# Optimization experiments

Measured on AMD Instinct MI355X. Metric: run time of the kernel, lower is better.

The kernel has to match this reference:

```python
import jax, jax.numpy as jnp
import numpy as np

N, F, B, T, K, C = 1000, 64, 16, 12, 5, 10
E = 16 * N
LN_EPS = 1e-5


def setup_inputs() -> dict:
    key = jax.random.key(0)
    ks = jax.random.split(key, 12)
    x = jax.random.normal(ks[0], (B, T, N, F), jnp.float32)
    # Edge list: ring guarantees every node has in-degree and out-degree >= 1
    # (DConv takes reciprocal of degrees), plus random edges to avg degree 16.
    rng = np.random.default_rng(0)
    ring = np.arange(N)
    src = np.concatenate([ring, rng.integers(0, N, E - N)])
    dst = np.concatenate([(ring + 1) % N, rng.integers(0, N, E - N)])
    edge_index = jnp.asarray(np.stack([src, dst]), jnp.int32)

    def winit(k, shape, fan):
        return (jax.random.normal(k, shape, jnp.float32) / np.sqrt(fan)).astype(jnp.float32)

    # DCRNN GRU cell = 3 diffusion convs, each on concat([X, H]) (2F in-channels)
    # DConv weight shape: (2 directions, K, in_channels, out_channels)
    W_z = winit(ks[1], (2, K, 2 * F, F), 2 * F)
    W_r = winit(ks[2], (2, K, 2 * F, F), 2 * F)
    W_h = winit(ks[3], (2, K, 2 * F, F), 2 * F)
    b_z = winit(ks[4], (F,), 100)
    b_r = winit(ks[5], (F,), 100)
    b_h = winit(ks[6], (F,), 100)
    ln_g = jnp.ones((F,), jnp.float32)
    ln_b = jnp.zeros((F,), jnp.float32)
    lin_w = winit(ks[7], (C, T * N * F), T * N * F)
    lin_b = winit(ks[8], (C,), 100)
    return {"x": x, "edge_index": edge_index, "W_z": W_z, "b_z": b_z,
            "W_r": W_r, "b_r": b_r, "W_h": W_h, "b_h": b_h,
            "ln_g": ln_g, "ln_b": ln_b, "lin_w": lin_w, "lin_b": lin_b}


def reference(x, edge_index, W_z, b_z, W_r, b_r, W_h, b_h, ln_g, ln_b, lin_w, lin_b):
    row, col = edge_index[0], edge_index[1]
    ones = jnp.ones(row.shape[0], x.dtype)
    deg_out = jax.ops.segment_sum(ones, row, num_segments=N)  # out-degree of src
    deg_in = jax.ops.segment_sum(ones, col, num_segments=N)   # in-degree (col sums)
    norm_out = (1.0 / deg_out)[row]  # per-edge 1/deg_out[src]
    norm_in = (1.0 / deg_in)[row]    # per-edge 1/deg_in[src] (src = target of reversed edge)

    def prop_out(h):  # out[dst] += h[src] / deg_out[src]
        return jax.ops.segment_sum(h[row] * norm_out[:, None], col, num_segments=N)

    def prop_in(h):   # reversed edges: out[src] += h[dst] / deg_in[src]
        return jax.ops.segment_sum(h[col] * norm_in[:, None], row, num_segments=N)

    def dconv(h, W, b):  # K-term Chebyshev diffusion conv, two directions
        Tx0 = h
        out = h @ W[0, 0] + h @ W[1, 0]
        Tx1o, Tx1i = prop_out(h), prop_in(h)
        out = out + Tx1o @ W[0, 1] + Tx1i @ W[1, 1]
        for k in range(2, K):
            Tx2o = 2.0 * prop_out(Tx1o) - Tx0
            Tx2i = 2.0 * prop_in(Tx1i) - Tx0
            out = out + Tx2o @ W[0, k] + Tx2i @ W[1, k]
            Tx0, Tx1o, Tx1i = Tx1o, Tx2o, Tx2i
        return out + b

    def cell(xs):  # xs: [N, F]; hidden state is None -> zeros for every snapshot
        h0 = jnp.zeros_like(xs)
        xh = jnp.concatenate([xs, h0], axis=1)
        z = jax.nn.sigmoid(dconv(xh, W_z, b_z))
        r = jax.nn.sigmoid(dconv(xh, W_r, b_r))
        xrh = jnp.concatenate([xs, r * h0], axis=1)
        h_tilde = jnp.tanh(dconv(xrh, W_h, b_h))
        return z * h0 + (1.0 - z) * h_tilde

    h = jax.vmap(cell)(x.reshape(B * T, N, F)).reshape(B, T, N, F)
    h = jax.nn.relu(h)  # dropout -> identity (eval mode)
    mu = jnp.mean(h, axis=-1, keepdims=True)
    var = jnp.mean((h - mu) ** 2, axis=-1, keepdims=True)
    h = (h - mu) / jnp.sqrt(var + LN_EPS) * ln_g + ln_b
    return h.reshape(B, -1) @ lin_w.T + lin_b
```

## Files before the change

kernel.cpp:

```cpp
#include <hip/hip_runtime.h>

#define NN   1000
#define EE   16000
#define FF   64
#define SS   192
#define TNF  768000
#define NB   16
#define NC   10
#define LWG2 1024
#define EPAD 24576

typedef unsigned short u16;
typedef unsigned int   u32;
typedef float f32x4_t __attribute__((ext_vector_type(4)));
typedef short s16x4_t __attribute__((ext_vector_type(4)));
typedef short s16x8_t __attribute__((ext_vector_type(8)));
typedef _Float16 f16x2_t __attribute__((ext_vector_type(2)));
typedef _Float16 f16x8_t __attribute__((ext_vector_type(8)));

__device__ __forceinline__ float bf2f(u16 u) {
    return __uint_as_float(((u32)u) << 16);
}
__device__ __forceinline__ u16 f2bf(float f) {
    u32 u = __float_as_uint(f);
    u32 r = u + 0x7FFFu + ((u >> 16) & 1u);
    return (u16)(r >> 16);
}
__device__ __forceinline__ u16 f2h(float f) {
    _Float16 h = (_Float16)f;
    return __builtin_bit_cast(unsigned short, h);
}
__device__ __forceinline__ float ldf(const void* p, size_t i, int f32m) {
    return f32m ? ((const float*)p)[i] : bf2f(((const u16*)p)[i]);
}

__device__ __forceinline__ uint2 pk4h(float4 v) {
    uint2 p;
    p.x = (u32)f2h(v.x) | ((u32)f2h(v.y) << 16);
    p.y = (u32)f2h(v.z) | ((u32)f2h(v.w) << 16);
    return p;
}

__device__ __forceinline__ void gl_lds16(const void* src, void* dst) {
    __builtin_amdgcn_global_load_lds(
        (const __attribute__((address_space(1))) unsigned int*)src,
        (__attribute__((address_space(3))) unsigned int*)dst, 16, 0, 0);
}

__global__ void k_pre(const u16* __restrict__ x, const int* __restrict__ ei,
                      int* __restrict__ flags, int* __restrict__ ints,
                      float* __restrict__ obuf, u16* __restrict__ eo_s,
                      u16* __restrict__ eid_s) {
    const int i = blockIdx.x * 256 + threadIdx.x;
    if (blockIdx.x == 0 && threadIdx.x < 64) {
        const int lane = threadIdx.x;
        u16 u1 = x[2 * lane], u2 = x[2 * (lane + 64)];
        int e1 = (u1 >> 7) & 0xFF, e2 = (u2 >> 7) & 0xFF;
        int ok1 = (u1 == 0 || (e1 >= 100 && e1 <= 140)) ? 1 : 0;
        int ok2 = (u2 == 0 || (e2 >= 100 && e2 <= 140)) ? 1 : 0;
        unsigned long long b1 = __ballot(ok1), b2 = __ballot(ok2);
        int nzf = (lane < 32 && ei[2 * lane + 1] != 0) ? 1 : 0;
        unsigned long long b3 = __ballot(nzf);
        if (lane == 0) {
            int good = __popcll(b1) + __popcll(b2);
            flags[0] = (good < 96) ? 1 : 0;
            flags[1] = (__popcll(b3) <= 4) ? 1 : 0;
        }
    }
    if (i < 4000) ints[i] = 0;
    if (i < 160) obuf[i] = 0.f;
    if (i < EPAD / 2) {
        ((u32*)eo_s)[i] = 0x1F401F40u;
        ((u32*)eid_s)[i] = 0x1F401F40u;
    }
}

__global__ void k_deg(const int* __restrict__ ei, int* __restrict__ deg,
                      const int* __restrict__ flags) {
    int e = blockIdx.x * 256 + threadIdx.x;
    const int sh = flags[1];
    if (e < EE) {
        int r = ei[(size_t)e << sh];
        int c = ei[(size_t)(EE + e) << sh];
        atomicAdd(&deg[r & 1023], 1);
        atomicAdd(&deg[NN + (c & 1023)], 1);
    }
}

__global__ __launch_bounds__(1024) void k_scan(const int* __restrict__ deg_in,
        const int* __restrict__ deg_out, int* __restrict__ ooffp, int* __restrict__ ioffp,
        float* __restrict__ inv_o, float* __restrict__ inv_i) {
    __shared__ int sa[1024], sb2[1024];
    const int t = threadIdx.x;
    for (int pass = 0; pass < 2; ++pass) {
        const int* deg = pass ? deg_out : deg_in;
        int* dst_off = pass ? ioffp : ooffp;
        sa[t] = (t < NN) ? ((deg[t] + 7) & ~7) : 0;
        __syncthreads();
        int* src = sa; int* dst = sb2;
        for (int offn = 1; offn < 1024; offn <<= 1) {
            int v = src[t];
            if (t >= offn) v += src[t - offn];
            dst[t] = v;
            __syncthreads();
            int* tmp = src; src = dst; dst = tmp;
        }
        if (t == 0) dst_off[0] = 0;
        if (t < NN) dst_off[t + 1] = src[t];
        __syncthreads();
    }
    if (t < NN) {
        inv_o[t] = 1.0f / (float)max(deg_out[t], 1);
        inv_i[t] = 1.0f / (float)max(deg_in[t], 1);
    }
}

__global__ void k_fill(const int* __restrict__ ei, const int* __restrict__ ooffp,
        const int* __restrict__ ioffp, int* __restrict__ cur,
        u16* __restrict__ eo_s, u16* __restrict__ eid_s,
        const int* __restrict__ flags) {
    int e = blockIdx.x * 256 + threadIdx.x;
    const int sh = flags[1];
    if (e < EE) {
        int r = ei[(size_t)e << sh] & 1023;
        int c = ei[(size_t)(EE + e) << sh] & 1023;
        int po = ooffp[c] + atomicAdd(&cur[c], 1);
        eo_s[po] = (u16)(r * 8);
        int pi = ioffp[r] + atomicAdd(&cur[NN + r], 1);
        eid_s[pi] = (u16)(c * 8);
    }
}

__global__ void k_wt(const void* __restrict__ Wz, const void* __restrict__ Wh,
                     u16* __restrict__ wt, const int* __restrict__ flags) {
    int idx = blockIdx.x * 256 + threadIdx.x;
    if (idx >= 128 * 576) return;
    const int f32m = flags[0];
    const int col = idx / 576;
    const int kk = idx - col * 576;
    const int j = kk >> 6, fi = kk & 63;
    const void* W = (col < 64) ? Wz : Wh;
    const int fo = col & 63;
    float v;
    if (j == 0) {
        v = ldf(W, (size_t)(0 * 128 + fi) * 64 + fo, f32m)
          + ldf(W, (size_t)(5 * 128 + fi) * 64 + fo, f32m);
    } else {
        const int d = (j & 1) ? 0 : 1;
        const int kq = (j + 1) >> 1;
        v = ldf(W, (size_t)((d * 5 + kq) * 128 + fi) * 64 + fo, f32m);
    }
    wt[col * 576 + kk] = f2h(v);
}


__device__ __forceinline__ float4 g8h(const char* __restrict__ S,
                                      const u16* __restrict__ lst, int e0, int e1) {
    f16x2_t a0 = {(_Float16)0, (_Float16)0}, a1 = a0, b0 = a0, b1 = a0;
    for (int e = e0; e < e1; e += 8) {
        uint4 w = *(const uint4*)(lst + e);
        int i0 = w.x & 0xFFFF, i1 = w.x >> 16;
        int i2 = w.y & 0xFFFF, i3 = w.y >> 16;
        int i4 = w.z & 0xFFFF, i5 = w.z >> 16;
        int i6 = w.w & 0xFFFF, i7 = w.w >> 16;
        uint2 q0 = *(const uint2*)(S + i0), q1 = *(const uint2*)(S + i1);
        uint2 q2 = *(const uint2*)(S + i2), q3 = *(const uint2*)(S + i3);
        uint2 q4 = *(const uint2*)(S + i4), q5 = *(const uint2*)(S + i5);
        uint2 q6 = *(const uint2*)(S + i6), q7 = *(const uint2*)(S + i7);
        a0 += __builtin_bit_cast(f16x2_t, q0.x); a1 += __builtin_bit_cast(f16x2_t, q0.y);
        b0 += __builtin_bit_cast(f16x2_t, q1.x); b1 += __builtin_bit_cast(f16x2_t, q1.y);
        a0 += __builtin_bit_cast(f16x2_t, q2.x); a1 += __builtin_bit_cast(f16x2_t, q2.y);
        b0 += __builtin_bit_cast(f16x2_t, q3.x); b1 += __builtin_bit_cast(f16x2_t, q3.y);
        a0 += __builtin_bit_cast(f16x2_t, q4.x); a1 += __builtin_bit_cast(f16x2_t, q4.y);
        b0 += __builtin_bit_cast(f16x2_t, q5.x); b1 += __builtin_bit_cast(f16x2_t, q5.y);
        a0 += __builtin_bit_cast(f16x2_t, q6.x); a1 += __builtin_bit_cast(f16x2_t, q6.y);
        b0 += __builtin_bit_cast(f16x2_t, q7.x); b1 += __builtin_bit_cast(f16x2_t, q7.y);
    }
    float4 r;
    r.x = (float)a0.x + (float)b0.x;
    r.y = (float)a0.y + (float)b0.y;
    r.z = (float)a1.x + (float)b1.x;
    r.w = (float)a1.y + (float)b1.y;
    return r;
}

__global__ __launch_bounds__(1024) void k_cheb(const void* __restrict__ xv_,
        const u16* __restrict__ eo_s, const int* __restrict__ ooffp,
        const u16* __restrict__ eid_s, const int* __restrict__ ioffp,
        const float* __restrict__ inv_o, const float* __restrict__ inv_i,
        u16* __restrict__ basis, int s0, int rchp,
        const int* __restrict__ flags, int chs) {
    __shared__ uint2 bXo[1024], bXi[1024], bA[1024], bB[1024];
    const int sb = blockIdx.x / chs;
    const int slocal = blockIdx.x - sb * chs;
    const int s = s0 + slocal;
    const int n = threadIdx.x;
    const bool act = (n < NN);
    const int f32m = flags[0];
    int e0o = 0, e1o = 0, e0i = 0, e1i = 0;
    float fiv = 0.f, fov = 0.f;
    const int row = slocal * NN + n;
    if (act) {
        e0o = ooffp[n]; e1o = ooffp[n + 1];
        e0i = ioffp[n]; e1i = ioffp[n + 1];
        fiv = inv_i[n];
        fov = inv_o[n];
    }
    const float fiv2 = 2.f * fiv;
    u16* const bp = basis + (size_t)(sb * 9) * rchp * 4 + (size_t)row * 4;
    const size_t jstep = (size_t)rchp * 4;
    float4 rx, rt1o, rt2o;
    if (n >= NN) {
        const uint2 z = make_uint2(0u, 0u);
        bXo[n] = z; bXi[n] = z; bA[n] = z; bB[n] = z;
    }
    if (act) {
        const size_t xoff = ((size_t)s * NN + n) * FF + sb * 4;
        if (f32m) {
            rx = *(const float4*)((const float*)xv_ + xoff);
        } else {
            ushort4 u = *(const ushort4*)((const u16*)xv_ + xoff);
            rx = make_float4(bf2f(u.x), bf2f(u.y), bf2f(u.z), bf2f(u.w));
        }
        bXi[n] = pk4h(rx);
        bXo[n] = pk4h(make_float4(fov * rx.x, fov * rx.y, fov * rx.z, fov * rx.w));
        *(uint2*)bp = pk4h(rx);
    }
    __syncthreads();
    if (act) {
        float4 go = g8h((const char*)bXo, eo_s, e0o, e1o);
        float4 gi = g8h((const char*)bXi, eid_s, e0i, e1i);
        rt1o = go;
        bA[n] = pk4h(make_float4(fov * go.x, fov * go.y, fov * go.z, fov * go.w));
        *(uint2*)(bp + jstep) = pk4h(go);
        float4 t = make_float4(gi.x * fiv, gi.y * fiv, gi.z * fiv, gi.w * fiv);
        bB[n] = pk4h(t);
        *(uint2*)(bp + 2 * jstep) = pk4h(t);
    }
    __syncthreads();
    if (act) {
        float4 go = g8h((const char*)bA, eo_s, e0o, e1o);
        float4 gi = g8h((const char*)bB, eid_s, e0i, e1i);
        float4 t2o = make_float4(fmaf(2.f, go.x, -rx.x), fmaf(2.f, go.y, -rx.y),
                                 fmaf(2.f, go.z, -rx.z), fmaf(2.f, go.w, -rx.w));
        rt2o = t2o;
        bXo[n] = pk4h(make_float4(fov * t2o.x, fov * t2o.y, fov * t2o.z, fov * t2o.w));
        *(uint2*)(bp + 3 * jstep) = pk4h(t2o);
        float4 t2i = make_float4(fmaf(fiv2, gi.x, -rx.x), fmaf(fiv2, gi.y, -rx.y),
                                 fmaf(fiv2, gi.z, -rx.z), fmaf(fiv2, gi.w, -rx.w));
        bXi[n] = pk4h(t2i);
        *(uint2*)(bp + 4 * jstep) = pk4h(t2i);
    }
    __syncthreads();
    if (act) {
        float4 go = g8h((const char*)bXo, eo_s, e0o, e1o);
        float4 gi = g8h((const char*)bXi, eid_s, e0i, e1i);
        float4 t3o = make_float4(fmaf(2.f, go.x, -rt1o.x), fmaf(2.f, go.y, -rt1o.y),
                                 fmaf(2.f, go.z, -rt1o.z), fmaf(2.f, go.w, -rt1o.w));
        bA[n] = pk4h(make_float4(fov * t3o.x, fov * t3o.y, fov * t3o.z, fov * t3o.w));
        *(uint2*)(bp + 5 * jstep) = pk4h(t3o);
        float4 t3i = make_float4(fmaf(fiv2, gi.x, -rt1o.x), fmaf(fiv2, gi.y, -rt1o.y),
                                 fmaf(fiv2, gi.z, -rt1o.z), fmaf(fiv2, gi.w, -rt1o.w));
        bB[n] = pk4h(t3i);
        *(uint2*)(bp + 6 * jstep) = pk4h(t3i);
    }
    __syncthreads();
    if (act) {
        float4 go = g8h((const char*)bA, eo_s, e0o, e1o);
        float4 gi = g8h((const char*)bB, eid_s, e0i, e1i);
        float4 t4o = make_float4(fmaf(2.f, go.x, -rt2o.x), fmaf(2.f, go.y, -rt2o.y),
                                 fmaf(2.f, go.z, -rt2o.z), fmaf(2.f, go.w, -rt2o.w));
        *(uint2*)(bp + 7 * jstep) = pk4h(t4o);
        float4 t4i = make_float4(fmaf(fiv2, gi.x, -rt2o.x), fmaf(fiv2, gi.y, -rt2o.y),
                                 fmaf(fiv2, gi.z, -rt2o.z), fmaf(fiv2, gi.w, -rt2o.w));
        *(uint2*)(bp + 8 * jstep) = pk4h(t4i);
    }
}


__global__ __launch_bounds__(256, 4) void k_gemm(const u16* __restrict__ basis,
        const u16* __restrict__ wt, const void* __restrict__ bz, const void* __restrict__ bh_,
        const void* __restrict__ lng, const void* __restrict__ lnb, u16* __restrict__ hnc,
        int rchp, int rchv, const int* __restrict__ flags) {
    union SM {
        struct { u16 A[2][4096]; u16 B[2][4096]; } st;
        float heh[128 * 65];
    };
    __shared__ SM sm;
    __shared__ float sMu[128], sRs[128];
    __shared__ float sBz[64], sBh[64], sG[64], sB2[64];

    const int tid = threadIdx.x;
    if (tid < 64) {
        const int f32m = flags[0];
        sBz[tid] = ldf(bz, tid, f32m); sBh[tid] = ldf(bh_, tid, f32m);
        sG[tid] = ldf(lng, tid, f32m); sB2[tid] = ldf(lnb, tid, f32m);
    }
    const int lane = tid & 63, wv = tid >> 6;
    const int wr = wv >> 1, wc = wv & 1;
    const int m = lane & 15, q = lane >> 4;
    const int r0 = blockIdx.x * 128;

    f32x4_t acc[4][4];
    const f32x4_t zero = {0.f, 0.f, 0.f, 0.f};
    for (int mi = 0; mi < 4; ++mi)
        for (int ni = 0; ni < 4; ++ni) acc[mi][ni] = zero;

    auto stage = [&](int bb, int t) {
        const int j = t >> 1, hf = t & 1;
        #pragma unroll
        for (int p = 0; p < 2; ++p) {
            int lin = p * 256 + tid;
            int sbp = lin >> 6, rp = lin & 63;
            const u16* src = basis + ((size_t)((hf * 8 + sbp) * 9 + j) * rchp + r0 + rp * 2) * 4;
            gl_lds16(src, &sm.st.A[bb][lin * 8]);
        }
        #pragma unroll
        for (int p = 0; p < 2; ++p) {
            int lin = p * 256 + tid;
            int c = lin >> 2;
            int qq = ((lin & 3) ^ c ^ (c >> 2)) & 3;
            gl_lds16(wt + c * 576 + t * 32 + qq * 8, &sm.st.B[bb][lin * 8]);
        }
    };

    stage(0, 0);
    for (int t = 0; t < 18; ++t) {
        const int bb = t & 1;
        __syncthreads();
        if (t + 1 < 18) stage(bb ^ 1, t + 1);
        s16x8_t af[4], bfr[4];
        #pragma unroll
        for (int mi = 0; mi < 4; ++mi) {
            int r = wr * 64 + mi * 16 + m;
            s16x4_t lo = *(const s16x4_t*)&sm.st.A[bb][(2 * q) * 512 + r * 4];
            s16x4_t hi = *(const s16x4_t*)&sm.st.A[bb][(2 * q + 1) * 512 + r * 4];
            af[mi] = __builtin_shufflevector(lo, hi, 0, 1, 2, 3, 4, 5, 6, 7);
        }
        #pragma unroll
        for (int ni = 0; ni < 4; ++ni) {
            int c = (ni < 2) ? (wc * 32 + ni * 16 + m) : (64 + wc * 32 + (ni - 2) * 16 + m);
            int slot = (q ^ c ^ (c >> 2)) & 3;
            bfr[ni] = *(const s16x8_t*)&sm.st.B[bb][(c * 4 + slot) * 8];
        }
        #pragma unroll
        for (int mi = 0; mi < 4; ++mi)
            #pragma unroll
            for (int ni = 0; ni < 4; ++ni)
                acc[mi][ni] = __builtin_amdgcn_mfma_f32_16x16x32_f16(
                    __builtin_bit_cast(f16x8_t, af[mi]),
                    __builtin_bit_cast(f16x8_t, bfr[ni]), acc[mi][ni], 0, 0, 0);
    }
    __syncthreads();

    #pragma unroll
    for (int mi = 0; mi < 4; ++mi) {
        #pragma unroll
        for (int ni = 0; ni < 2; ++ni) {
            const int f = wc * 32 + ni * 16 + m;
            const float vbz = sBz[f], vbh = sBh[f];
            #pragma unroll
            for (int r = 0; r < 4; ++r) {
                const int rl = wr * 64 + mi * 16 + q * 4 + r;
                float zp = acc[mi][ni][r];
                float hp = acc[mi][ni + 2][r];
                zp = (zp == zp) ? zp : 0.f;
                hp = (hp == hp) ? hp : 0.f;
                zp = fminf(fmaxf(zp + vbz, -30.f), 30.f);
                hp = fminf(fmaxf(hp + vbh, -15.f), 15.f);
                const float z = __fdividef(1.f, 1.f + __expf(-zp));
                const float e2 = __expf(2.f * hp);
                const float ht = __fdividef(e2 - 1.f, e2 + 1.f);
                float h = (1.f - z) * ht;
                h = fmaxf(h, 0.f);
                sm.heh[rl * 65 + f] = h;
            }
        }
    }
    __syncthreads();
    if (tid < 128) {
        float sum = 0.f, ss = 0.f;
        #pragma unroll 8
        for (int f = 0; f < 64; ++f) {
            float v = sm.heh[tid * 65 + f];
            sum += v; ss += v * v;
        }
        float mu = sum * 0.015625f;
        float var = fmaxf(ss * 0.015625f - mu * mu, 0.f);
        sMu[tid] = mu;
        sRs[tid] = rsqrtf(var + 1e-5f);
    }
    __syncthreads();
    for (int idx = tid; idx < 128 * 64; idx += 256) {
        int rl = idx >> 6, f = idx & 63;
        if (r0 + rl < rchv) {
            float v = (sm.heh[rl * 65 + f] - sMu[rl]) * sRs[rl] * sG[f] + sB2[f];
            hnc[(size_t)(r0 + rl) * 64 + f] = f2bf(v);
        }
    }
}


__global__ __launch_bounds__(256) void k_lin_chunk(const u16* __restrict__ hnc,
        const void* __restrict__ lw, float* __restrict__ obuf, int s0, int chs,
        const int* __restrict__ flags) {
    const int tid = threadIdx.x;
    const int f32m = flags[0];
    float acc[NB][NC];
    #pragma unroll
    for (int b = 0; b < NB; ++b)
        #pragma unroll
        for (int c = 0; c < NC; ++c) acc[b][c] = 0.f;

    const int hi_s = s0 + chs - 1;
    for (int w = blockIdx.x * 256 + tid; w < TNF; w += LWG2 * 256) {
        const int t = w / 64000;
        int blo_n = s0 - t + 11;
        const int blo = (blo_n > 0) ? (blo_n / 12) : 0;
        const int bhi_n = hi_s - t;
        const int bhi = (bhi_n >= 0) ? (bhi_n / 12) : -1;
        if (bhi < blo) continue;
        float wvv[NC];
        if (f32m) {
            #pragma unroll
            for (int c = 0; c < NC; ++c) wvv[c] = ((const float*)lw)[(size_t)c * TNF + w];
        } else {
            #pragma unroll
            for (int c = 0; c < NC; ++c) wvv[c] = bf2f(((const u16*)lw)[(size_t)c * TNF + w]);
        }
        #pragma unroll
        for (int c = 0; c < NC; ++c) {
            float v = wvv[c];
            wvv[c] = (v == v && v > -1e30f && v < 1e30f) ? v : 0.f;
        }
        #pragma unroll
        for (int b = 0; b < NB; ++b) {
            if (b >= blo && b <= bhi) {
                const int sl = b * 12 + t - s0;
                const float h = bf2f(hnc[(size_t)sl * 64000 + (w - t * 64000)]);
                #pragma unroll
                for (int c = 0; c < NC; ++c) acc[b][c] = fmaf(h, wvv[c], acc[b][c]);
            }
        }
    }
    __shared__ float sRed[4][160];
    const int wvi = tid >> 6, lane = tid & 63;
    #pragma unroll
    for (int b = 0; b < NB; ++b)
        #pragma unroll
        for (int c = 0; c < NC; ++c) {
            float v = acc[b][c];
            #pragma unroll
            for (int off = 1; off < 64; off <<= 1) v += __shfl_xor(v, off, 64);
            if (lane == 0) sRed[wvi][b * NC + c] = v;
        }
    __syncthreads();
    if (tid < 160)
        atomicAdd(&obuf[tid], sRed[0][tid] + sRed[1][tid] + sRed[2][tid] + sRed[3][tid]);
}

__global__ void k_red(const float* __restrict__ obuf, const void* __restrict__ lb,
                      void* __restrict__ out, const int* __restrict__ flags) {
    const int o = threadIdx.x;
    const int f32m = flags[0];
    if (o < 160) {
        float s = obuf[o] + ldf(lb, o % NC, f32m);
        if (f32m) ((float*)out)[o] = s;
        else      ((u16*)out)[o] = f2bf(s);
    }
}


extern "C" void kernel_launch(void* const* d_in, const int* in_sizes, int n_in,
                              void* d_out, int out_size, void* d_ws, size_t ws_size,
                              hipStream_t stream) {
    (void)in_sizes; (void)n_in; (void)out_size;
    const void* x   = d_in[0];
    const int*  ei  = (const int*)d_in[1];
    const void* Wz  = d_in[2];
    const void* bz  = d_in[3];
    const void* Wh  = d_in[6];
    const void* bh  = d_in[7];
    const void* lng = d_in[8];
    const void* lnb = d_in[9];
    const void* lw  = d_in[10];
    const void* lb  = d_in[11];

    char* ws = (char*)d_ws;
    size_t off = 0;
    auto alloc = [&](size_t bytes) -> void* {
        void* p = ws + off;
        off = (off + bytes + 255) & ~(size_t)255;
        return p;
    };
    int*   flags    = (int*)  alloc(64);
    u16*   wt       = (u16*)  alloc(128 * 576 * 2);
    int*   ints     = (int*)  alloc(4000 * 4);
    int*   ooffp    = (int*)  alloc(1024 * 4);
    int*   ioffp    = (int*)  alloc(1024 * 4);
    float* inv_o    = (float*)alloc(1000 * 4);
    float* inv_i    = (float*)alloc(1000 * 4);
    u16*   eo_s     = (u16*)  alloc((size_t)EPAD * 2);
    u16*   eid_s    = (u16*)  alloc((size_t)EPAD * 2);
    float* obuf     = (float*)alloc(160 * 4);

    const int cand[] = {192, 96, 64, 48, 32, 24, 16, 12, 8, 6, 4, 3, 2, 1};
    int CHS = 1, RCHP = 1024;
    for (int ci = 0; ci < 14; ++ci) {
        int c = cand[ci];
        int rchp = ((c * NN + 127) / 128) * 128;
        size_t need = (size_t)16 * 9 * rchp * 8 + (size_t)c * NN * FF * 2 + 8192;
        if (off + need <= ws_size) { CHS = c; RCHP = rchp; break; }
    }
    u16* basis = (u16*)alloc((size_t)16 * 9 * RCHP * 8);
    u16* hnc   = (u16*)alloc((size_t)CHS * NN * FF * 2);

    int* deg_out = ints;
    int* deg_in  = ints + 1000;
    int* cur     = ints + 2000;

    k_pre<<<160, 256, 0, stream>>>((const u16*)x, ei, flags, ints, obuf, eo_s, eid_s);
    k_deg<<<(EE + 255) / 256, 256, 0, stream>>>(ei, ints, flags);
    k_scan<<<1, 1024, 0, stream>>>(deg_in, deg_out, ooffp, ioffp, inv_o, inv_i);
    k_fill<<<(EE + 255) / 256, 256, 0, stream>>>(ei, ooffp, ioffp, cur, eo_s, eid_s, flags);
    k_wt<<<288, 256, 0, stream>>>(Wz, Wh, wt, flags);
    const int nchunk = SS / CHS;
    for (int ch = 0; ch < nchunk; ++ch) {
        k_cheb<<<CHS * 16, 1024, 0, stream>>>(x, eo_s, ooffp, eid_s, ioffp, inv_o, inv_i,
                                              basis, ch * CHS, RCHP, flags, CHS);
        k_gemm<<<RCHP / 128, 256, 0, stream>>>(basis, wt, bz, bh, lng, lnb, hnc,
                                               RCHP, CHS * NN, flags);
        k_lin_chunk<<<LWG2, 256, 0, stream>>>(hnc, lw, obuf, ch * CHS, CHS, flags);
    }
    k_red<<<1, 256, 0, stream>>>(obuf, lb, d_out, flags);
}
```

Baseline: 483.0 us.

## Restructure final linear kernel to one block per snapshot slice with vector loads

The final linear projection kernel now assigns each block one snapshot and one eighth of its feature row, instead of a fixed grid striding over all weights with per-element batch-range checks. Each thread loads eight bf16 activations and eight weights per class with 128-bit vector loads, keeping only 10 accumulators instead of 160. This removes the scalar loads, the divergent batch loop and the large register footprint. In exchange, weight rows are re-read for every batch sample in the chunk rather than shared across samples.

```diff
diff --git a/kernel.cpp b/kernel.cpp
--- a/kernel.cpp
+++ b/kernel.cpp
@@ -7,7 +7,7 @@
 #define TNF  768000
 #define NB   16
 #define NC   10
-#define LWG2 1024
+#define LSPL 8
 #define EPAD 24576
 
 typedef unsigned short u16;
@@ -401,62 +401,78 @@
 }
 
 
-__global__ __launch_bounds__(256) void k_lin_chunk(const u16* __restrict__ hnc,
+__global__ __launch_bounds__(256) void k_lin(const u16* __restrict__ hnc,
         const void* __restrict__ lw, float* __restrict__ obuf, int s0, int chs,
         const int* __restrict__ flags) {
+    const int sl = blockIdx.x / LSPL;
+    const int q  = blockIdx.x - sl * LSPL;
+    const int s  = s0 + sl;
+    const int b  = s / 12, t = s - b * 12;
     const int tid = threadIdx.x;
     const int f32m = flags[0];
-    float acc[NB][NC];
+    const int base = q * 8000;
+    const u16* hrow = hnc + (size_t)sl * 64000 + base;
+    const size_t lwoff = (size_t)t * 64000 + base;
+
+    float acc[NC];
     #pragma unroll
-    for (int b = 0; b < NB; ++b)
-        #pragma unroll
-        for (int c = 0; c < NC; ++c) acc[b][c] = 0.f;
-
-    const int hi_s = s0 + chs - 1;
-    for (int w = blockIdx.x * 256 + tid; w < TNF; w += LWG2 * 256) {
-        const int t = w / 64000;
-        int blo_n = s0 - t + 11;
-        const int blo = (blo_n > 0) ? (blo_n / 12) : 0;
-        const int bhi_n = hi_s - t;
-        const int bhi = (bhi_n >= 0) ? (bhi_n / 12) : -1;
-        if (bhi < blo) continue;
-        float wvv[NC];
-        if (f32m) {
+    for (int c = 0; c < NC; ++c) acc[c] = 0.f;
+
+    #pragma unroll
+    for (int it = 0; it < 4; ++it) {
+        const int p = tid + it * 256;
+        if (p < 1000) {
+            const int w8 = p * 8;
+            uint4 hv = *(const uint4*)(hrow + w8);
+            float h0 = bf2f((u16)(hv.x & 0xFFFF)), h1 = bf2f((u16)(hv.x >> 16));
+            float h2 = bf2f((u16)(hv.y & 0xFFFF)), h3 = bf2f((u16)(hv.y >> 16));
+            float h4 = bf2f((u16)(hv.z & 0xFFFF)), h5 = bf2f((u16)(hv.z >> 16));
+            float h6 = bf2f((u16)(hv.w & 0xFFFF)), h7 = bf2f((u16)(hv.w >> 16));
             #pragma unroll
-            for (int c = 0; c < NC; ++c) wvv[c] = ((const float*)lw)[(size_t)c * TNF + w];
-        } else {
-            #pragma unroll
-            for (int c = 0; c < NC; ++c) wvv[c] = bf2f(((const u16*)lw)[(size_t)c * TNF + w]);
-        }
-        #pragma unroll
-        for (int c = 0; c < NC; ++c) {
-            float v = wvv[c];
-            wvv[c] = (v == v && v > -1e30f && v < 1e30f) ? v : 0.f;
-        }
-        #pragma unroll
-        for (int b = 0; b < NB; ++b) {
-            if (b >= blo && b <= bhi) {
-                const int sl = b * 12 + t - s0;
-                const float h = bf2f(hnc[(size_t)sl * 64000 + (w - t * 64000)]);
-                #pragma unroll
-                for (int c = 0; c < NC; ++c) acc[b][c] = fmaf(h, wvv[c], acc[b][c]);
+            for (int c = 0; c < NC; ++c) {
+                float v0, v1, v2, v3, v4, v5, v6, v7;
+                if (f32m) {
+                    const float* lp = (const float*)lw + (size_t)c * TNF + lwoff + w8;
+                    float4 a = *(const float4*)lp;
+                    float4 bv = *(const float4*)(lp + 4);
+                    v0 = a.x; v1 = a.y; v2 = a.z; v3 = a.w;
+                    v4 = bv.x; v5 = bv.y; v6 = bv.z; v7 = bv.w;
+                } else {
+                    const u16* lp = (const u16*)lw + (size_t)c * TNF + lwoff + w8;
+                    uint4 a = *(const uint4*)lp;
+                    v0 = bf2f((u16)(a.x & 0xFFFF)); v1 = bf2f((u16)(a.x >> 16));
+                    v2 = bf2f((u16)(a.y & 0xFFFF)); v3 = bf2f((u16)(a.y >> 16));
+                    v4 = bf2f((u16)(a.z & 0xFFFF)); v5 = bf2f((u16)(a.z >> 16));
+                    v6 = bf2f((u16)(a.w & 0xFFFF)); v7 = bf2f((u16)(a.w >> 16));
+                }
+                v0 = (v0 == v0 && v0 > -1e30f && v0 < 1e30f) ? v0 : 0.f;
+                v1 = (v1 == v1 && v1 > -1e30f && v1 < 1e30f) ? v1 : 0.f;
+                v2 = (v2 == v2 && v2 > -1e30f && v2 < 1e30f) ? v2 : 0.f;
+                v3 = (v3 == v3 && v3 > -1e30f && v3 < 1e30f) ? v3 : 0.f;
+                v4 = (v4 == v4 && v4 > -1e30f && v4 < 1e30f) ? v4 : 0.f;
+                v5 = (v5 == v5 && v5 > -1e30f && v5 < 1e30f) ? v5 : 0.f;
+                v6 = (v6 == v6 && v6 > -1e30f && v6 < 1e30f) ? v6 : 0.f;
+                v7 = (v7 == v7 && v7 > -1e30f && v7 < 1e30f) ? v7 : 0.f;
+                float a0 = fmaf(h0, v0, fmaf(h1, v1, fmaf(h2, v2, h3 * v3)));
+                float a1 = fmaf(h4, v4, fmaf(h5, v5, fmaf(h6, v6, h7 * v7)));
+                acc[c] += a0 + a1;
             }
         }
     }
-    __shared__ float sRed[4][160];
+
+    __shared__ float sRed[4][NC];
     const int wvi = tid >> 6, lane = tid & 63;
     #pragma unroll
-    for (int b = 0; b < NB; ++b)
-        #pragma unroll
-        for (int c = 0; c < NC; ++c) {
-            float v = acc[b][c];
-            #pragma unroll
-            for (int off = 1; off < 64; off <<= 1) v += __shfl_xor(v, off, 64);
-            if (lane == 0) sRed[wvi][b * NC + c] = v;
-        }
-    __syncthreads();
-    if (tid < 160)
-        atomicAdd(&obuf[tid], sRed[0][tid] + sRed[1][tid] + sRed[2][tid] + sRed[3][tid]);
+    for (int c = 0; c < NC; ++c) {
+        float v = acc[c];
+        #pragma unroll
+        for (int off = 1; off < 64; off <<= 1) v += __shfl_xor(v, off, 64);
+        if (lane == 0) sRed[wvi][c] = v;
+    }
+    __syncthreads();
+    if (tid < NC)
+        atomicAdd(&obuf[b * NC + tid],
+                  sRed[0][tid] + sRed[1][tid] + sRed[2][tid] + sRed[3][tid]);
 }
 
 __global__ void k_red(const float* __restrict__ obuf, const void* __restrict__ lb,
@@ -530,7 +546,7 @@
                                               basis, ch * CHS, RCHP, flags, CHS);
         k_gemm<<<RCHP / 128, 256, 0, stream>>>(basis, wt, bz, bh, lng, lnb, hnc,
                                                RCHP, CHS * NN, flags);
-        k_lin_chunk<<<LWG2, 256, 0, stream>>>(hnc, lw, obuf, ch * CHS, CHS, flags);
+        k_lin<<<CHS * LSPL, 256, 0, stream>>>(hnc, lw, obuf, ch * CHS, CHS, flags);
     }
     k_red<<<1, 256, 0, stream>>>(obuf, lb, d_out, flags);
 }
```

New measurement: 401.7 us. 1.2x faster.

## Fuse final linear projection into GEMM epilogue and drop hnc buffer

Applied to the files above, without the earlier changes.

The layernormed hidden state is no longer written to an intermediate bf16 buffer and reread by a separate linear kernel. Each GEMM block now multiplies its own normalized rows against the matching slice of the linear weights and atomically adds per-batch partial sums into the output accumulator. A per-row index table handles rows that cross a batch boundary, up to two batches per block. The cheb kernel launch is also split into two half-grid launches with a sub-block offset, which may only change scheduling.

```diff
diff --git a/kernel.cpp b/kernel.cpp
--- a/kernel.cpp
+++ b/kernel.cpp
@@ -7,7 +7,6 @@
 #define TNF  768000
 #define NB   16
 #define NC   10
-#define LWG2 1024
 #define EPAD 24576
 
 typedef unsigned short u16;
@@ -189,10 +188,10 @@
         const u16* __restrict__ eid_s, const int* __restrict__ ioffp,
         const float* __restrict__ inv_o, const float* __restrict__ inv_i,
         u16* __restrict__ basis, int s0, int rchp,
-        const int* __restrict__ flags, int chs) {
+        const int* __restrict__ flags, int chs, int sbo) {
     __shared__ uint2 bXo[1024], bXi[1024], bA[1024], bB[1024];
-    const int sb = blockIdx.x / chs;
-    const int slocal = blockIdx.x - sb * chs;
+    const int sb = sbo + blockIdx.x / chs;
+    const int slocal = blockIdx.x - (sb - sbo) * chs;
     const int s = s0 + slocal;
     const int n = threadIdx.x;
     const bool act = (n < NN);
@@ -280,8 +279,9 @@
 
 __global__ __launch_bounds__(256, 4) void k_gemm(const u16* __restrict__ basis,
         const u16* __restrict__ wt, const void* __restrict__ bz, const void* __restrict__ bh_,
-        const void* __restrict__ lng, const void* __restrict__ lnb, u16* __restrict__ hnc,
-        int rchp, int rchv, const int* __restrict__ flags) {
+        const void* __restrict__ lng, const void* __restrict__ lnb,
+        const void* __restrict__ lw, float* __restrict__ obuf,
+        int rchp, int rchv, int s0, const int* __restrict__ flags) {
     union SM {
         struct { u16 A[2][4096]; u16 B[2][4096]; } st;
         float heh[128 * 65];
@@ -289,10 +289,12 @@
     __shared__ SM sm;
     __shared__ float sMu[128], sRs[128];
     __shared__ float sBz[64], sBh[64], sG[64], sB2[64];
+    __shared__ u32 sRI[128];
+    __shared__ float sRed[4][20];
 
     const int tid = threadIdx.x;
+    const int f32m = flags[0];
     if (tid < 64) {
-        const int f32m = flags[0];
         sBz[tid] = ldf(bz, tid, f32m); sBh[tid] = ldf(bh_, tid, f32m);
         sG[tid] = ldf(lng, tid, f32m); sB2[tid] = ldf(lnb, tid, f32m);
     }
@@ -300,6 +302,18 @@
     const int wr = wv >> 1, wc = wv & 1;
     const int m = lane & 15, q = lane >> 4;
     const int r0 = blockIdx.x * 128;
+    const int bLo = (s0 + r0 / 1000) / 12;
+    if (tid < 128) {
+        int row = r0 + tid;
+        u32 ri = 0xFFFFFFFFu;
+        if (row < rchv) {
+            int slocal = row / 1000;
+            int s = s0 + slocal;
+            int b = s / 12, t = s - b * 12, n = row - slocal * 1000;
+            ri = ((u32)(b != bLo) << 24) | (u32)(t * 64000 + n * 64);
+        }
+        sRI[tid] = ri;
+    }
 
     f32x4_t acc[4][4];
     const f32x4_t zero = {0.f, 0.f, 0.f, 0.f};
@@ -391,72 +405,72 @@
         sRs[tid] = rsqrtf(var + 1e-5f);
     }
     __syncthreads();
-    for (int idx = tid; idx < 128 * 64; idx += 256) {
-        int rl = idx >> 6, f = idx & 63;
-        if (r0 + rl < rchv) {
-            float v = (sm.heh[rl * 65 + f] - sMu[rl]) * sRs[rl] * sG[f] + sB2[f];
-            hnc[(size_t)(r0 + rl) * 64 + f] = f2bf(v);
-        }
-    }
-}
-
-
-__global__ __launch_bounds__(256) void k_lin_chunk(const u16* __restrict__ hnc,
-        const void* __restrict__ lw, float* __restrict__ obuf, int s0, int chs,
-        const int* __restrict__ flags) {
-    const int tid = threadIdx.x;
-    const int f32m = flags[0];
-    float acc[NB][NC];
+
+    float facc[2][NC];
     #pragma unroll
-    for (int b = 0; b < NB; ++b)
-        #pragma unroll
-        for (int c = 0; c < NC; ++c) acc[b][c] = 0.f;
-
-    const int hi_s = s0 + chs - 1;
-    for (int w = blockIdx.x * 256 + tid; w < TNF; w += LWG2 * 256) {
-        const int t = w / 64000;
-        int blo_n = s0 - t + 11;
-        const int blo = (blo_n > 0) ? (blo_n / 12) : 0;
-        const int bhi_n = hi_s - t;
-        const int bhi = (bhi_n >= 0) ? (bhi_n / 12) : -1;
-        if (bhi < blo) continue;
-        float wvv[NC];
-        if (f32m) {
+    for (int hb = 0; hb < 2; ++hb)
+        #pragma unroll
+        for (int c = 0; c < NC; ++c) facc[hb][c] = 0.f;
+    #pragma unroll
+    for (int it = 0; it < 4; ++it) {
+        const int rl = (tid >> 3) + it * 32;
+        const int f8 = (tid & 7) * 8;
+        const u32 ri = sRI[rl];
+        if (ri != 0xFFFFFFFFu) {
+            const int hb = (ri >> 24) & 1;
+            const u32 wb = ri & 0xFFFFFu;
+            const float mu = sMu[rl], rs = sRs[rl];
+            float v[8];
             #pragma unroll
-            for (int c = 0; c < NC; ++c) wvv[c] = ((const float*)lw)[(size_t)c * TNF + w];
-        } else {
+            for (int k = 0; k < 8; ++k)
+                v[k] = (sm.heh[rl * 65 + f8 + k] - mu) * rs * sG[f8 + k] + sB2[f8 + k];
             #pragma unroll
-            for (int c = 0; c < NC; ++c) wvv[c] = bf2f(((const u16*)lw)[(size_t)c * TNF + w]);
-        }
-        #pragma unroll
-        for (int c = 0; c < NC; ++c) {
-            float v = wvv[c];
-            wvv[c] = (v == v && v > -1e30f && v < 1e30f) ? v : 0.f;
-        }
-        #pragma unroll
-        for (int b = 0; b < NB; ++b) {
-            if (b >= blo && b <= bhi) {
-                const int sl = b * 12 + t - s0;
-                const float h = bf2f(hnc[(size_t)sl * 64000 + (w - t * 64000)]);
-                #pragma unroll
-                for (int c = 0; c < NC; ++c) acc[b][c] = fmaf(h, wvv[c], acc[b][c]);
+            for (int c = 0; c < NC; ++c) {
+                float w0, w1, w2, w3, w4, w5, w6, w7;
+                if (f32m) {
+                    const float* lp = (const float*)lw + (size_t)c * TNF + wb + f8;
+                    float4 a = *(const float4*)lp;
+                    float4 b4 = *(const float4*)(lp + 4);
+                    w0 = a.x; w1 = a.y; w2 = a.z; w3 = a.w;
+                    w4 = b4.x; w5 = b4.y; w6 = b4.z; w7 = b4.w;
+                } else {
+                    const u16* lp = (const u16*)lw + (size_t)c * TNF + wb + f8;
+                    uint4 a = *(const uint4*)lp;
+                    w0 = bf2f((u16)(a.x & 0xFFFF)); w1 = bf2f((u16)(a.x >> 16));
+                    w2 = bf2f((u16)(a.y & 0xFFFF)); w3 = bf2f((u16)(a.y >> 16));
+                    w4 = bf2f((u16)(a.z & 0xFFFF)); w5 = bf2f((u16)(a.z >> 16));
+                    w6 = bf2f((u16)(a.w & 0xFFFF)); w7 = bf2f((u16)(a.w >> 16));
+                }
+                w0 = (w0 == w0 && w0 > -1e30f && w0 < 1e30f) ? w0 : 0.f;
+                w1 = (w1 == w1 && w1 > -1e30f && w1 < 1e30f) ? w1 : 0.f;
+                w2 = (w2 == w2 && w2 > -1e30f && w2 < 1e30f) ? w2 : 0.f;
+                w3 = (w3 == w3 && w3 > -1e30f && w3 < 1e30f) ? w3 : 0.f;
+                w4 = (w4 == w4 && w4 > -1e30f && w4 < 1e30f) ? w4 : 0.f;
+                w5 = (w5 == w5 && w5 > -1e30f && w5 < 1e30f) ? w5 : 0.f;
+                w6 = (w6 == w6 && w6 > -1e30f && w6 < 1e30f) ? w6 : 0.f;
+                w7 = (w7 == w7 && w7 > -1e30f && w7 < 1e30f) ? w7 : 0.f;
+                float a0 = fmaf(v[0], w0, fmaf(v[1], w1, fmaf(v[2], w2, v[3] * w3)));
+                float a1 = fmaf(v[4], w4, fmaf(v[5], w5, fmaf(v[6], w6, v[7] * w7)));
+                if (hb) facc[1][c] += a0 + a1; else facc[0][c] += a0 + a1;
             }
         }
     }
-    __shared__ float sRed[4][160];
-    const int wvi = tid >> 6, lane = tid & 63;
     #pragma unroll
-    for (int b = 0; b < NB; ++b)
-        #pragma unroll
-        for (int c = 0; c < NC; ++c) {
-            float v = acc[b][c];
-            #pragma unroll
-            for (int off = 1; off < 64; off <<= 1) v += __shfl_xor(v, off, 64);
-            if (lane == 0) sRed[wvi][b * NC + c] = v;
-        }
-    __syncthreads();
-    if (tid < 160)
-        atomicAdd(&obuf[tid], sRed[0][tid] + sRed[1][tid] + sRed[2][tid] + sRed[3][tid]);
+    for (int j = 0; j < 20; ++j) {
+        float val = facc[j / 10][j % 10];
+        #pragma unroll
+        for (int off = 1; off < 64; off <<= 1) val += __shfl_xor(val, off, 64);
+        if (lane == 0) sRed[wv][j] = val;
+    }
+    __syncthreads();
+    if (tid < 20) {
+        const int hb = tid / 10, c = tid - hb * 10;
+        const int bo = bLo + hb;
+        if (bo < NB) {
+            float sum = sRed[0][tid] + sRed[1][tid] + sRed[2][tid] + sRed[3][tid];
+            atomicAdd(&obuf[bo * NC + c], sum);
+        }
+    }
 }
 
 __global__ void k_red(const float* __restrict__ obuf, const void* __restrict__ lb,
@@ -509,11 +523,10 @@
     for (int ci = 0; ci < 14; ++ci) {
         int c = cand[ci];
         int rchp = ((c * NN + 127) / 128) * 128;
-        size_t need = (size_t)16 * 9 * rchp * 8 + (size_t)c * NN * FF * 2 + 8192;
+        size_t need = (size_t)16 * 9 * rchp * 8 + 8192;
         if (off + need <= ws_size) { CHS = c; RCHP = rchp; break; }
     }
     u16* basis = (u16*)alloc((size_t)16 * 9 * RCHP * 8);
-    u16* hnc   = (u16*)alloc((size_t)CHS * NN * FF * 2);
 
     int* deg_out = ints;
     int* deg_in  = ints + 1000;
@@ -526,11 +539,12 @@
     k_wt<<<288, 256, 0, stream>>>(Wz, Wh, wt, flags);
     const int nchunk = SS / CHS;
     for (int ch = 0; ch < nchunk; ++ch) {
-        k_cheb<<<CHS * 16, 1024, 0, stream>>>(x, eo_s, ooffp, eid_s, ioffp, inv_o, inv_i,
-                                              basis, ch * CHS, RCHP, flags, CHS);
-        k_gemm<<<RCHP / 128, 256, 0, stream>>>(basis, wt, bz, bh, lng, lnb, hnc,
-                                               RCHP, CHS * NN, flags);
-        k_lin_chunk<<<LWG2, 256, 0, stream>>>(hnc, lw, obuf, ch * CHS, CHS, flags);
+        k_cheb<<<CHS * 8, 1024, 0, stream>>>(x, eo_s, ooffp, eid_s, ioffp, inv_o, inv_i,
+                                             basis, ch * CHS, RCHP, flags, CHS, 0);
+        k_cheb<<<CHS * 8, 1024, 0, stream>>>(x, eo_s, ooffp, eid_s, ioffp, inv_o, inv_i,
+                                             basis, ch * CHS, RCHP, flags, CHS, 8);
+        k_gemm<<<RCHP / 128, 256, 0, stream>>>(basis, wt, bz, bh, lng, lnb, lw, obuf,
+                                               RCHP, CHS * NN, ch * CHS, flags);
     }
     k_red<<<1, 256, 0, stream>>>(obuf, lb, d_out, flags);
 }
```

After: 439.4 us. 1.1x faster.
